# Optimization experiments

Measured on AMD Instinct MI355X. Metric: run time of the kernel, lower is better.

Reference implementation:

```python
import jax, jax.numpy as jnp
import numpy as np

C, PE, L, HEADS = 256, 64, 6, 4
N_GRAPHS, S = 2048, 64            # uniform graphs of S nodes -> dense batch is a reshape
N = N_GRAPHS * S                  # 131072 nodes
E = N * 4                         # 524288 edges
BN_EPS = 1e-5


def _bn(h, g, b):
    # BatchNorm1d, training-mode statistics (biased variance), affine
    m = h.mean(0)
    v = h.var(0)
    return (h - m) / jnp.sqrt(v + BN_EPS) * g + b


def setup_inputs() -> dict:
    key = jax.random.key(0)
    ks = iter(jax.random.split(key, 64))
    def rn(shape, scale=0.05):
        return jax.random.normal(next(ks), shape, dtype=jnp.float32) * scale
    x = jax.random.randint(next(ks), (N, 1), 0, 28)
    pe = jax.random.normal(next(ks), (N, 20), dtype=jnp.float32)
    epg = E // N_GRAPHS
    base = (jnp.arange(E) // epg) * S          # edges stay within their graph
    src = base + jax.random.randint(next(ks), (E,), 0, S)
    dst = base + jax.random.randint(next(ks), (E,), 0, S)
    edge_index = jnp.stack([src, dst])
    edge_attr = jax.random.randint(next(ks), (E,), 0, 4)
    batch = jnp.arange(N) // S
    return dict(
        x=x, pe=pe, edge_index=edge_index, edge_attr=edge_attr, batch=batch,
        node_emb=rn((28, C - PE), 1.0), pe_lin_w=rn((20, PE)), pe_lin_b=jnp.zeros(PE),
        pe_norm_g=jnp.ones(20), pe_norm_b=jnp.zeros(20),
        edge_emb=rn((4, C), 1.0),
        conv_w1=rn((L, C, C)), conv_b1=jnp.zeros((L, C)),
        conv_w2=rn((L, C, C)), conv_b2=jnp.zeros((L, C)),
        attn_in_w=rn((L, C, 3 * C)), attn_in_b=jnp.zeros((L, 3 * C)),
        attn_out_w=rn((L, C, C)), attn_out_b=jnp.zeros((L, C)),
        bn1_g=jnp.ones((L, C)), bn1_b=jnp.zeros((L, C)),
        bn2_g=jnp.ones((L, C)), bn2_b=jnp.zeros((L, C)),
        bn3_g=jnp.ones((L, C)), bn3_b=jnp.zeros((L, C)),
        mlp_w1=rn((L, C, 2 * C)), mlp_b1=jnp.zeros((L, 2 * C)),
        mlp_w2=rn((L, 2 * C, C)), mlp_b2=jnp.zeros((L, C)),
        head_w1=rn((C, C // 2)), head_b1=jnp.zeros(C // 2),
        head_w2=rn((C // 2, C // 4)), head_b2=jnp.zeros(C // 4),
        head_w3=rn((C // 4, 1)), head_b3=jnp.zeros(1),
    )


def reference(x, pe, edge_index, edge_attr, batch, node_emb, pe_lin_w, pe_lin_b,
              pe_norm_g, pe_norm_b, edge_emb, conv_w1, conv_b1, conv_w2, conv_b2,
              attn_in_w, attn_in_b, attn_out_w, attn_out_b,
              bn1_g, bn1_b, bn2_g, bn2_b, bn3_g, bn3_b,
              mlp_w1, mlp_b1, mlp_w2, mlp_b2,
              head_w1, head_b1, head_w2, head_b2, head_w3, head_b3):
    x_pe = _bn(pe, pe_norm_g, pe_norm_b)
    h = jnp.concatenate([node_emb[x[:, 0]], x_pe @ pe_lin_w + pe_lin_b], axis=1)  # [N, C]
    ea = edge_emb[edge_attr]                                                      # [E, C]
    src, dst = edge_index[0], edge_index[1]
    d = C // HEADS
    scale = 1.0 / jnp.sqrt(jnp.float32(d))
    for l in range(L):
        # --- local GINEConv: nn((1+eps)*x_i + sum_j relu(x_j + e_ij)), eps=0 ---
        msg = jax.nn.relu(h[src] + ea)                          # gather + add + relu
        aggr = jax.ops.segment_sum(msg, dst, num_segments=N)    # scatter-add
        z = h + aggr
        hl = jax.nn.relu(z @ conv_w1[l] + conv_b1[l]) @ conv_w2[l] + conv_b2[l]
        hl = _bn(hl + h, bn1_g[l], bn1_b[l])                    # residual + norm1
        # --- global multihead attention on dense batch [G, S, C] ---
        hd = h.reshape(N_GRAPHS, S, C)
        qkv = hd @ attn_in_w[l] + attn_in_b[l]
        q, k, v = jnp.split(qkv, 3, axis=-1)
        q = q.reshape(N_GRAPHS, S, HEADS, d).transpose(0, 2, 1, 3)
        k = k.reshape(N_GRAPHS, S, HEADS, d).transpose(0, 2, 1, 3)
        v = v.reshape(N_GRAPHS, S, HEADS, d).transpose(0, 2, 1, 3)
        a = jax.nn.softmax(jnp.einsum('ghqd,ghkd->ghqk', q, k) * scale, axis=-1)
        o = jnp.einsum('ghqk,ghkd->ghqd', a, v).transpose(0, 2, 1, 3).reshape(N_GRAPHS, S, C)
        o = (o @ attn_out_w[l] + attn_out_b[l]).reshape(N, C)
        ha = _bn(o + h, bn2_g[l], bn2_b[l])                     # residual + norm2
        # --- combine + FFN ---
        out = hl + ha
        ff = jax.nn.relu(out @ mlp_w1[l] + mlp_b1[l]) @ mlp_w2[l] + mlp_b2[l]
        h = _bn(out + ff, bn3_g[l], bn3_b[l])                   # residual + norm3
    pooled = jax.ops.segment_sum(h, batch, num_segments=N_GRAPHS)  # global_add_pool -> [G, C]
    t = jax.nn.relu(pooled @ head_w1 + head_b1)
    t = jax.nn.relu(t @ head_w2 + head_b2)
    return t @ head_w3 + head_b3                                   # [G, 1]
```

## Files before the change

kernel.cpp:

```cpp
#include <hip/hip_runtime.h>

#define N_NODES 131072
#define N_EDGES 524288
#define CCH 256
#define N_GRAPHS_ 2048
#define SEQ 64
#define LAYERS 6

typedef unsigned short US;
typedef __attribute__((ext_vector_type(8))) short v8s;
typedef __attribute__((ext_vector_type(8))) unsigned short v8us;
typedef __attribute__((ext_vector_type(4))) float v4f;

__device__ __forceinline__ float b2f(US u) { return __uint_as_float(((unsigned)u) << 16); }
__device__ __forceinline__ US f2b(float f) {
    unsigned u = __float_as_uint(f);
    return (US)((u + 0x7fff + ((u >> 16) & 1)) >> 16);
}

__device__ float g_stats[512];
__device__ float g_aff1[512];
__device__ float g_aff2[512];
__device__ float g_aff3[512];
__device__ float g_pe[40];
__device__ float g_peaff[40];
__device__ US    g_wt[6 * 655360];
__device__ int   g_csr[N_EDGES];
__device__ int   g_off[N_GRAPHS_ * 65];

__global__ __launch_bounds__(256) void wt_k(const float* __restrict__ cw1, const float* __restrict__ cw2,
                                            const float* __restrict__ aiw, const float* __restrict__ aow,
                                            const float* __restrict__ mw1, const float* __restrict__ mw2) {
    __shared__ float t[64][65];
    int b = blockIdx.x;
    int l = b / 160, r = b % 160;
    const float* src; int ldw, ldk, ctiles; size_t doff;
    if (r < 16)      { src = cw1 + (size_t)l * 65536;  ldw = 256; ldk = 256; ctiles = 4;  doff = 0;      }
    else if (r < 32) { src = cw2 + (size_t)l * 65536;  ldw = 256; ldk = 256; ctiles = 4;  doff = 65536;  r -= 16; }
    else if (r < 80) { src = aiw + (size_t)l * 196608; ldw = 768; ldk = 256; ctiles = 12; doff = 131072; r -= 32; }
    else if (r < 96) { src = aow + (size_t)l * 65536;  ldw = 256; ldk = 256; ctiles = 4;  doff = 327680; r -= 80; }
    else if (r < 128){ src = mw1 + (size_t)l * 131072; ldw = 512; ldk = 256; ctiles = 8;  doff = 393216; r -= 96; }
    else             { src = mw2 + (size_t)l * 131072; ldw = 256; ldk = 512; ctiles = 4;  doff = 524288; r -= 128; }
    int kt = r / ctiles, ct = r % ctiles;
    int k0 = kt * 64, c0 = ct * 64;
    US* dst = g_wt + (size_t)l * 655360 + doff;
    int tid = threadIdx.x;
    int rr = tid >> 4, c4 = (tid & 15) * 4;
    #pragma unroll
    for (int j = 0; j < 4; j++) {
        float4 v = *(const float4*)(src + (size_t)(k0 + rr + j * 16) * ldw + c0 + c4);
        t[rr + j * 16][c4 + 0] = v.x; t[rr + j * 16][c4 + 1] = v.y;
        t[rr + j * 16][c4 + 2] = v.z; t[rr + j * 16][c4 + 3] = v.w;
    }
    __syncthreads();
    #pragma unroll
    for (int j = 0; j < 4; j++) {
        int crow = rr + j * 16;
        ushort4 o;
        o.x = f2b(t[c4 + 0][crow]); o.y = f2b(t[c4 + 1][crow]);
        o.z = f2b(t[c4 + 2][crow]); o.w = f2b(t[c4 + 3][crow]);
        *(ushort4*)(dst + (size_t)(c0 + crow) * ldk + k0 + c4) = o;
    }
}

__global__ __launch_bounds__(256) void csr_k(const int* __restrict__ ei,
                                             const int* __restrict__ attr) {
    __shared__ int deg[64], off[65];
    int g = blockIdx.x, tid = threadIdx.x;
    if (tid < 64) deg[tid] = 0;
    __syncthreads();
    int e = g * 256 + tid;
    int d = ei[N_EDGES + e] - g * 64;
    int slot = atomicAdd(&deg[d], 1);
    __syncthreads();
    if (tid == 0) {
        off[0] = 0;
        for (int i = 0; i < 64; i++) off[i + 1] = off[i] + deg[i];
    }
    __syncthreads();
    g_csr[g * 256 + off[d] + slot] = (ei[e] - g * 64) | (attr[e] << 6);
    if (tid < 65) g_off[g * 65 + tid] = off[tid];
}

__global__ __launch_bounds__(256) void pe_part_k(const float* __restrict__ pe) {
    __shared__ float red[240], red2[240];
    int b = blockIdx.x, tid = threadIdx.x;
    float s = 0.f, s2 = 0.f;
    if (tid < 240) {
        int ch = tid % 20, sub = tid / 20;
        size_t r0 = (size_t)b * 512;
        for (int r = sub; r < 512; r += 12) {
            float v = pe[(r0 + r) * 20 + ch];
            s += v; s2 += v * v;
        }
        red[tid] = s; red2[tid] = s2;
    }
    __syncthreads();
    if (tid < 20) {
        float ts = 0.f, ts2 = 0.f;
        #pragma unroll
        for (int sub = 0; sub < 12; sub++) { ts += red[sub * 20 + tid]; ts2 += red2[sub * 20 + tid]; }
        atomicAdd(&g_pe[tid], ts);
        atomicAdd(&g_pe[20 + tid], ts2);
    }
}

__global__ __launch_bounds__(64) void pe_fin_k(const float* __restrict__ g,
                                               const float* __restrict__ b) {
    int t = threadIdx.x;
    if (t < 20) {
        float mean = g_pe[t] / (float)N_NODES;
        float var  = g_pe[20 + t] / (float)N_NODES - mean * mean;
        float a = g[t] * rsqrtf(var + 1e-5f);
        g_peaff[t] = a;
        g_peaff[20 + t] = b[t] - mean * a;
        g_pe[t] = 0.f;
        g_pe[20 + t] = 0.f;
    }
}

__global__ __launch_bounds__(256) void embed_k(const int* __restrict__ x,
                                               const float* __restrict__ pe,
                                               const float* __restrict__ node_emb,
                                               const float* __restrict__ plw,
                                               const float* __restrict__ plb,
                                               US* __restrict__ h) {
    int n = blockIdx.x;
    int tid = threadIdx.x;
    int xi = x[n];
    float v;
    if (tid < 192) {
        v = node_emb[xi * 192 + tid];
    } else {
        int j = tid - 192;
        float s = plb[j];
        #pragma unroll
        for (int k = 0; k < 20; k++) {
            float p = pe[(size_t)n * 20 + k] * g_peaff[k] + g_peaff[20 + k];
            s += p * plw[k * 64 + j];
        }
        v = s;
    }
    h[(size_t)n * CCH + tid] = f2b(v);
}

__global__ __launch_bounds__(256) void aggr_z_k(const US* __restrict__ h,
                                                const float* __restrict__ eemb,
                                                US* __restrict__ z) {
    __shared__ US ht[64 * 264];
    __shared__ float em[4 * 260];
    __shared__ int off[65], ce[256];
    int g = blockIdx.x, tid = threadIdx.x;
    for (int v = tid; v < 2048; v += 256) {
        int row = v >> 5, seg = (v & 31) * 8;
        *(v8us*)&ht[row * 264 + seg] = *(const v8us*)(h + (size_t)(g * 64 + row) * 256 + seg);
    }
    for (int i = tid; i < 1024; i += 256)
        em[(i >> 8) * 260 + (i & 255)] = eemb[(i >> 8) * 256 + (i & 255)];
    ce[tid] = g_csr[g * 256 + tid];
    if (tid < 65) off[tid] = g_off[g * 65 + tid];
    __syncthreads();

    int dst = tid >> 2, cq = (tid & 3) * 4;
    float acc[64];
    #pragma unroll
    for (int i = 0; i < 64; i++) acc[i] = 0.f;
    int e1 = off[dst + 1];
    for (int e = off[dst]; e < e1; e++) {
        int val = ce[e];
        int src = val & 63, a = (val >> 6) & 3;
        #pragma unroll
        for (int i = 0; i < 16; i++) {
            int c = cq + i * 16;
            ushort4 hv = *(ushort4*)&ht[src * 264 + c];
            float4 ev = *(float4*)&em[a * 260 + c];
            acc[i * 4 + 0] += fmaxf(b2f(hv.x) + ev.x, 0.f);
            acc[i * 4 + 1] += fmaxf(b2f(hv.y) + ev.y, 0.f);
            acc[i * 4 + 2] += fmaxf(b2f(hv.z) + ev.z, 0.f);
            acc[i * 4 + 3] += fmaxf(b2f(hv.w) + ev.w, 0.f);
        }
    }
    US* zp = z + (size_t)(g * 64 + dst) * 256;
    #pragma unroll
    for (int i = 0; i < 16; i++) {
        int c = cq + i * 16;
        ushort4 hv = *(ushort4*)&ht[dst * 264 + c];
        ushort4 o;
        o.x = f2b(b2f(hv.x) + acc[i * 4 + 0]);
        o.y = f2b(b2f(hv.y) + acc[i * 4 + 1]);
        o.z = f2b(b2f(hv.z) + acc[i * 4 + 2]);
        o.w = f2b(b2f(hv.w) + acc[i * 4 + 3]);
        *(ushort4*)(zp + c) = o;
    }
}

template<int NG, bool STATS>
__global__ __launch_bounds__(256, 2) void gemm_mfma_k(const US* __restrict__ A,
                                                      size_t woff, int ldk,
                                                      int w0, int w1, int w2, int w3,
                                                      const float* __restrict__ bias,
                                                      const US* __restrict__ res,
                                                      US* __restrict__ Y, int mode) {
    const US* __restrict__ Wt = g_wt + woff;
    __shared__ __align__(16) US As[128 * 40];
    __shared__ __align__(16) US Bs[NG * 64 * 40];
    int tid = threadIdx.x;
    size_t row0 = (size_t)blockIdx.x * 128;
    int w = tid >> 6, l = tid & 63;

    int sb_c = tid >> 2, sb_ko = (tid & 3) * 8;
    int a_off0 = (w * 32 + (l & 15)) * 40 + (l >> 4) * 8;
    int a_off1 = a_off0 + 16 * 40;
    int b_off  = (l & 15) * 40 + (l >> 4) * 8;

    const US* aptr0 = A + (row0 + sb_c) * 256 + sb_ko;
    const US* aptr1 = aptr0 + 64 * 256;

    v4f acc[2][NG * 4];
    #pragma unroll
    for (int i = 0; i < 2; i++)
        #pragma unroll
        for (int t = 0; t < NG * 4; t++) acc[i][t] = (v4f){0.f, 0.f, 0.f, 0.f};

    v8us pa0 = *(const v8us*)aptr0;
    v8us pa1 = *(const v8us*)aptr1;
    v8us pb[NG];
    #pragma unroll
    for (int p = 0; p < NG; p++) {
        int wb = (p == 0) ? w0 : (p == 1) ? w1 : (p == 2) ? w2 : w3;
        pb[p] = *(const v8us*)(Wt + (size_t)(wb + sb_c) * ldk + sb_ko);
    }

    for (int kc = 0; kc < 8; kc++) {
        *(v8us*)&As[sb_c * 40 + sb_ko] = pa0;
        *(v8us*)&As[(sb_c + 64) * 40 + sb_ko] = pa1;
        #pragma unroll
        for (int p = 0; p < NG; p++)
            *(v8us*)&Bs[(p * 64 + sb_c) * 40 + sb_ko] = pb[p];
        __syncthreads();
        if (kc < 7) {
            int kn = (kc + 1) * 32;
            pa0 = *(const v8us*)(aptr0 + kn);
            pa1 = *(const v8us*)(aptr1 + kn);
            #pragma unroll
            for (int p = 0; p < NG; p++) {
                int wb = (p == 0) ? w0 : (p == 1) ? w1 : (p == 2) ? w2 : w3;
                pb[p] = *(const v8us*)(Wt + (size_t)(wb + sb_c) * ldk + kn + sb_ko);
            }
        }
        v8s a0 = *(v8s*)&As[a_off0];
        v8s a1 = *(v8s*)&As[a_off1];
        #pragma unroll
        for (int t = 0; t < NG * 4; t++) {
            v8s bf = *(v8s*)&Bs[b_off + t * 640];
            acc[0][t] = __builtin_amdgcn_mfma_f32_16x16x32_bf16(a0, bf, acc[0][t], 0, 0, 0);
            acc[1][t] = __builtin_amdgcn_mfma_f32_16x16x32_bf16(a1, bf, acc[1][t], 0, 0, 0);
        }
        __syncthreads();
    }

    int col_l = l & 15;
    int rs = (l >> 4) * 4;
    float cs[NG * 4], cs2[NG * 4];
    if (STATS) {
        #pragma unroll
        for (int t = 0; t < NG * 4; t++) { cs[t] = 0.f; cs2[t] = 0.f; }
    }
    #pragma unroll
    for (int i = 0; i < 2; i++) {
        #pragma unroll
        for (int t = 0; t < NG * 4; t++) {
            int grp = t >> 2;
            int wb = (grp == 0) ? w0 : (grp == 1) ? w1 : (grp == 2) ? w2 : w3;
            int c = t * 16 + col_l;
            float bv = bias ? bias[wb + (t & 3) * 16 + col_l] : 0.f;
            #pragma unroll
            for (int r = 0; r < 4; r++) {
                size_t rr = row0 + w * 32 + i * 16 + rs + r;
                float v = acc[i][t][r] + bv;
                if (mode == 1) v = fmaxf(v, 0.f);
                if (mode == 2) v += b2f(res[rr * 256 + c]);
                if (STATS) { cs[t] += v; cs2[t] += v * v; }
                Y[rr * 256 + c] = f2b(v);
            }
        }
    }
    if (STATS) {
        #pragma unroll
        for (int t = 0; t < NG * 4; t++) {
            cs[t]  += __shfl_xor(cs[t], 16);  cs[t]  += __shfl_xor(cs[t], 32);
            cs2[t] += __shfl_xor(cs2[t], 16); cs2[t] += __shfl_xor(cs2[t], 32);
        }
        float* sred = (float*)As;
        if ((l >> 4) == 0) {
            #pragma unroll
            for (int t = 0; t < NG * 4; t++) {
                sred[w * 256 + t * 16 + col_l] = cs[t];
                sred[1024 + w * 256 + t * 16 + col_l] = cs2[t];
            }
        }
        __syncthreads();
        int c = tid;
        if (c < NG * 64) {
            float s  = sred[c] + sred[256 + c] + sred[512 + c] + sred[768 + c];
            float s2 = sred[1024 + c] + sred[1280 + c] + sred[1536 + c] + sred[1792 + c];
            atomicAdd(&g_stats[c], s);
            atomicAdd(&g_stats[CCH + c], s2);
        }
    }
}

__global__ __launch_bounds__(64) void attn_k(const US* __restrict__ qkv,
                                             US* __restrict__ o) {
    __shared__ __align__(16) US Ps[64 * 72];
    __shared__ __align__(16) US Vt[64 * 72];
    int g = blockIdx.x, l = threadIdx.x;
    int li = l & 15, hi8 = (l >> 4) * 8, hi4 = (l >> 4) * 4;
    const US* base = qkv + (size_t)g * 64 * 256;

    {
        v8us vv[8];
        #pragma unroll
        for (int jv = 0; jv < 8; jv++)
            vv[jv] = *(const v8us*)(base + l * 256 + 128 + jv * 8);
        #pragma unroll
        for (int jv = 0; jv < 8; jv++)
            #pragma unroll
            for (int e = 0; e < 8; e++)
                Vt[(jv * 8 + e) * 72 + l] = vv[jv][e];
    }

    v8s Qf[4][2], Kf[4][2];
    #pragma unroll
    for (int t = 0; t < 4; t++)
        #pragma unroll
        for (int ds = 0; ds < 2; ds++) {
            Qf[t][ds] = *(const v8s*)(base + (t * 16 + li) * 256 + ds * 32 + hi8);
            Kf[t][ds] = *(const v8s*)(base + (t * 16 + li) * 256 + 64 + ds * 32 + hi8);
        }

    v4f S[4][4];
    #pragma unroll
    for (int qt = 0; qt < 4; qt++)
        #pragma unroll
        for (int kt = 0; kt < 4; kt++) {
            v4f a = (v4f){0.f, 0.f, 0.f, 0.f};
            a = __builtin_amdgcn_mfma_f32_16x16x32_bf16(Qf[qt][0], Kf[kt][0], a, 0, 0, 0);
            a = __builtin_amdgcn_mfma_f32_16x16x32_bf16(Qf[qt][1], Kf[kt][1], a, 0, 0, 0);
            S[qt][kt] = a;
        }

    #pragma unroll
    for (int qt = 0; qt < 4; qt++)
        #pragma unroll
        for (int r = 0; r < 4; r++) {
            float mx = -1e30f;
            #pragma unroll
            for (int kt = 0; kt < 4; kt++) {
                S[qt][kt][r] *= 0.125f;
                mx = fmaxf(mx, S[qt][kt][r]);
            }
            mx = fmaxf(mx, __shfl_xor(mx, 1));
            mx = fmaxf(mx, __shfl_xor(mx, 2));
            mx = fmaxf(mx, __shfl_xor(mx, 4));
            mx = fmaxf(mx, __shfl_xor(mx, 8));
            float sum = 0.f;
            #pragma unroll
            for (int kt = 0; kt < 4; kt++) {
                float e = __expf(S[qt][kt][r] - mx);
                S[qt][kt][r] = e;
                sum += e;
            }
            sum += __shfl_xor(sum, 1);
            sum += __shfl_xor(sum, 2);
            sum += __shfl_xor(sum, 4);
            sum += __shfl_xor(sum, 8);
            float inv = 1.f / sum;
            #pragma unroll
            for (int kt = 0; kt < 4; kt++)
                Ps[(qt * 16 + hi4 + r) * 72 + kt * 16 + li] = f2b(S[qt][kt][r] * inv);
        }

    v4f O[4][4];
    #pragma unroll
    for (int qt = 0; qt < 4; qt++)
        #pragma unroll
        for (int jt = 0; jt < 4; jt++) O[qt][jt] = (v4f){0.f, 0.f, 0.f, 0.f};
    #pragma unroll
    for (int ks = 0; ks < 2; ks++) {
        v8s Pf[4], Vf[4];
        #pragma unroll
        for (int qt = 0; qt < 4; qt++)
            Pf[qt] = *(v8s*)&Ps[(qt * 16 + li) * 72 + ks * 32 + hi8];
        #pragma unroll
        for (int jt = 0; jt < 4; jt++)
            Vf[jt] = *(v8s*)&Vt[(jt * 16 + li) * 72 + ks * 32 + hi8];
        #pragma unroll
        for (int qt = 0; qt < 4; qt++)
            #pragma unroll
            for (int jt = 0; jt < 4; jt++)
                O[qt][jt] = __builtin_amdgcn_mfma_f32_16x16x32_bf16(Pf[qt], Vf[jt], O[qt][jt], 0, 0, 0);
    }

    #pragma unroll
    for (int qt = 0; qt < 4; qt++)
        #pragma unroll
        for (int jt = 0; jt < 4; jt++)
            #pragma unroll
            for (int r = 0; r < 4; r++)
                Ps[(qt * 16 + hi4 + r) * 72 + jt * 16 + li] = f2b(O[qt][jt][r]);
    US* ob = o + (size_t)(g * 64 + l) * 256;
    #pragma unroll
    for (int jv = 0; jv < 8; jv++)
        *(v8us*)(ob + jv * 8) = *(v8us*)&Ps[l * 72 + jv * 8];
}

__global__ __launch_bounds__(256) void affine_k(const float* __restrict__ g,
                                                const float* __restrict__ b, int sel) {
    int c = threadIdx.x;
    float mean = g_stats[c] / (float)N_NODES;
    float var  = g_stats[CCH + c] / (float)N_NODES - mean * mean;
    float a = g[c] * rsqrtf(var + 1e-5f);
    float* dst = (sel == 0) ? g_aff1 : (sel == 1) ? g_aff2 : g_aff3;
    dst[c] = a;
    dst[CCH + c] = b[c] - mean * a;
    g_stats[c] = 0.f;
    g_stats[CCH + c] = 0.f;
}

__global__ __launch_bounds__(256) void combine_k(const US* __restrict__ y1,
                                                 const US* __restrict__ y2,
                                                 US* __restrict__ out) {
    size_t idx = (size_t)blockIdx.x * 256 + threadIdx.x;
    size_t stride = (size_t)gridDim.x * 256;
    for (; idx < (size_t)N_NODES * CCH / 8; idx += stride) {
        size_t i = idx * 8;
        int c = (int)(i & 255);
        v8us a = *(const v8us*)(y1 + i);
        v8us b = *(const v8us*)(y2 + i);
        v8us o;
        #pragma unroll
        for (int j = 0; j < 8; j++) {
            float v = b2f(a[j]) * g_aff1[c + j] + g_aff1[CCH + c + j] +
                      b2f(b[j]) * g_aff2[c + j] + g_aff2[CCH + c + j];
            o[j] = f2b(v);
        }
        *(v8us*)(out + i) = o;
    }
}

__global__ __launch_bounds__(256) void apply_k(US* __restrict__ h) {
    size_t idx = (size_t)blockIdx.x * 256 + threadIdx.x;
    size_t stride = (size_t)gridDim.x * 256;
    for (; idx < (size_t)N_NODES * CCH / 8; idx += stride) {
        size_t i = idx * 8;
        int c = (int)(i & 255);
        v8us a = *(const v8us*)(h + i);
        v8us o;
        #pragma unroll
        for (int j = 0; j < 8; j++)
            o[j] = f2b(b2f(a[j]) * g_aff3[c + j] + g_aff3[CCH + c + j]);
        *(v8us*)(h + i) = o;
    }
}

__global__ __launch_bounds__(256) void pool_k(const US* __restrict__ h,
                                              float* __restrict__ pooled) {
    int g = blockIdx.x, c = threadIdx.x;
    float s = 0.f;
    for (int ss = 0; ss < SEQ; ss++) s += b2f(h[((size_t)g * SEQ + ss) * CCH + c]);
    pooled[(size_t)g * CCH + c] = s;
}

__global__ __launch_bounds__(128) void head_k(const float* __restrict__ pooled,
                                              const float* __restrict__ w1, const float* __restrict__ b1,
                                              const float* __restrict__ w2, const float* __restrict__ b2,
                                              const float* __restrict__ w3, const float* __restrict__ b3,
                                              float* __restrict__ outp) {
    __shared__ float p[256], t1[128], t2[64];
    int g = blockIdx.x, tid = threadIdx.x;
    p[tid] = pooled[(size_t)g * CCH + tid];
    p[tid + 128] = pooled[(size_t)g * CCH + 128 + tid];
    __syncthreads();
    float s = b1[tid];
    for (int k = 0; k < 256; k++) s += p[k] * w1[k * 128 + tid];
    t1[tid] = fmaxf(s, 0.f);
    __syncthreads();
    if (tid < 64) {
        float s2 = b2[tid];
        for (int k = 0; k < 128; k++) s2 += t1[k] * w2[k * 64 + tid];
        t2[tid] = fmaxf(s2, 0.f);
    }
    __syncthreads();
    if (tid == 0) {
        float s3 = b3[0];
        for (int k = 0; k < 64; k++) s3 += t2[k] * w3[k];
        outp[g] = s3;
    }
}

extern "C" void kernel_launch(void* const* d_in, const int* in_sizes, int n_in,
                              void* d_out, int out_size, void* d_ws, size_t ws_size,
                              hipStream_t stream) {
    const int*   x         = (const int*)  d_in[0];
    const float* pe        = (const float*)d_in[1];
    const int*   ei        = (const int*)  d_in[2];
    const int*   eattr     = (const int*)  d_in[3];
    const float* node_emb  = (const float*)d_in[5];
    const float* pe_lin_w  = (const float*)d_in[6];
    const float* pe_lin_b  = (const float*)d_in[7];
    const float* pe_norm_g = (const float*)d_in[8];
    const float* pe_norm_b = (const float*)d_in[9];
    const float* edge_emb  = (const float*)d_in[10];
    const float* conv_w1   = (const float*)d_in[11];
    const float* conv_b1   = (const float*)d_in[12];
    const float* conv_w2   = (const float*)d_in[13];
    const float* conv_b2   = (const float*)d_in[14];
    const float* attn_in_w = (const float*)d_in[15];
    const float* attn_in_b = (const float*)d_in[16];
    const float* attn_out_w= (const float*)d_in[17];
    const float* attn_out_b= (const float*)d_in[18];
    const float* bn1_g     = (const float*)d_in[19];
    const float* bn1_b     = (const float*)d_in[20];
    const float* bn2_g     = (const float*)d_in[21];
    const float* bn2_b     = (const float*)d_in[22];
    const float* bn3_g     = (const float*)d_in[23];
    const float* bn3_b     = (const float*)d_in[24];
    const float* mlp_w1    = (const float*)d_in[25];
    const float* mlp_b1    = (const float*)d_in[26];
    const float* mlp_w2    = (const float*)d_in[27];
    const float* mlp_b2    = (const float*)d_in[28];
    const float* head_w1   = (const float*)d_in[29];
    const float* head_b1   = (const float*)d_in[30];
    const float* head_w2   = (const float*)d_in[31];
    const float* head_b2   = (const float*)d_in[32];
    const float* head_w3   = (const float*)d_in[33];
    const float* head_b3   = (const float*)d_in[34];
    (void)in_sizes; (void)n_in; (void)out_size; (void)ws_size;

    char* ws = (char*)d_ws;
    US* h = (US*)(ws);
    US* A = (US*)(ws + 67108864ULL);
    US* B = (US*)(ws + 134217728ULL);
    US* C = (US*)(ws + 201326592ULL);
    float* pooled = (float*)(ws + 67108864ULL);

    wt_k<<<960, 256, 0, stream>>>(conv_w1, conv_w2, attn_in_w, attn_out_w, mlp_w1, mlp_w2);
    csr_k<<<N_GRAPHS_, 256, 0, stream>>>(ei, eattr);
    pe_part_k<<<256, 256, 0, stream>>>(pe);
    pe_fin_k<<<1, 64, 0, stream>>>(pe_norm_g, pe_norm_b);
    embed_k<<<N_NODES, 256, 0, stream>>>(x, pe, node_emb, pe_lin_w, pe_lin_b, h);

    for (int l = 0; l < LAYERS; l++) {
        size_t wl = (size_t)l * 655360;

        aggr_z_k<<<N_GRAPHS_, 256, 0, stream>>>(h, edge_emb, A);
        gemm_mfma_k<4, false><<<1024, 256, 0, stream>>>(A, wl, 256, 0, 64, 128, 192,
                                                        conv_b1 + l * 256, nullptr, B, 1);
        gemm_mfma_k<4, true><<<1024, 256, 0, stream>>>(B, wl + 65536, 256, 0, 64, 128, 192,
                                                       conv_b2 + l * 256, h, C, 2);
        affine_k<<<1, 256, 0, stream>>>(bn1_g + l * 256, bn1_b + l * 256, 0);

        for (int hh = 0; hh < 4; hh++) {
            gemm_mfma_k<3, false><<<1024, 256, 0, stream>>>(h, wl + 131072, 256,
                                                            hh * 64, 256 + hh * 64, 512 + hh * 64, 0,
                                                            attn_in_b + l * 768, nullptr, A, 0);
            attn_k<<<N_GRAPHS_, 64, 0, stream>>>(A, B + hh * 64);
        }
        gemm_mfma_k<4, true><<<1024, 256, 0, stream>>>(B, wl + 327680, 256, 0, 64, 128, 192,
                                                       attn_out_b + l * 256, h, h, 2);
        affine_k<<<1, 256, 0, stream>>>(bn2_g + l * 256, bn2_b + l * 256, 1);

        combine_k<<<2048, 256, 0, stream>>>(C, h, A);
        gemm_mfma_k<4, false><<<1024, 256, 0, stream>>>(A, wl + 393216, 256, 0, 64, 128, 192,
                                                        mlp_b1 + l * 512, nullptr, B, 1);
        gemm_mfma_k<4, false><<<1024, 256, 0, stream>>>(B, wl + 524288, 512, 0, 64, 128, 192,
                                                        mlp_b2 + l * 256, A, C, 2);
        gemm_mfma_k<4, false><<<1024, 256, 0, stream>>>(A, wl + 393216, 256, 256, 320, 384, 448,
                                                        mlp_b1 + l * 512, nullptr, B, 1);
        gemm_mfma_k<4, true><<<1024, 256, 0, stream>>>(B, wl + 524288 + 256, 512, 0, 64, 128, 192,
                                                       nullptr, C, h, 2);
        affine_k<<<1, 256, 0, stream>>>(bn3_g + l * 256, bn3_b + l * 256, 2);
        apply_k<<<2048, 256, 0, stream>>>(h);
    }

    pool_k<<<N_GRAPHS_, 256, 0, stream>>>(h, pooled);
    head_k<<<N_GRAPHS_, 128, 0, stream>>>(pooled, head_w1, head_b1, head_w2, head_b2,
                                          head_w3, head_b3, (float*)d_out);
}
```

Baseline: 5.743 ms.

## Double-buffer GEMM tiles via direct global-to-LDS loads and stage epilogue through LDS

The MFMA GEMM kernel now fills swizzled, double-buffered LDS tiles with global_load_lds, so the next K-chunk loads while the current one computes, with no register round trip. The epilogue writes accumulators to LDS and re-reads them row-wise, giving coalesced 16-byte output and residual accesses. BatchNorm column statistics are now computed from the LDS-staged values. The cost is more barriers in the epilogue and a larger LDS footprint, which could limit occupancy. The stats path assumes all 256 columns are valid, so it only matches the old behaviour when NG is 4.

```diff
diff --git a/kernel.cpp b/kernel.cpp
--- a/kernel.cpp
+++ b/kernel.cpp
@@ -16,6 +16,11 @@
 __device__ __forceinline__ US f2b(float f) {
     unsigned u = __float_as_uint(f);
     return (US)((u + 0x7fff + ((u >> 16) & 1)) >> 16);
+}
+__device__ __forceinline__ void gload16(const US* g, US* l) {
+    __builtin_amdgcn_global_load_lds(
+        (const __attribute__((address_space(1))) unsigned int*)g,
+        (__attribute__((address_space(3))) unsigned int*)l, 16, 0, 0);
 }
 
 __device__ float g_stats[512];
@@ -202,19 +207,24 @@
                                                       const US* __restrict__ res,
                                                       US* __restrict__ Y, int mode) {
     const US* __restrict__ Wt = g_wt + woff;
-    __shared__ __align__(16) US As[128 * 40];
-    __shared__ __align__(16) US Bs[NG * 64 * 40];
+    __shared__ __align__(16) char smem[16384 + 2 * NG * 4096];
+    US* As0 = (US*)smem;
+    US* As1 = (US*)(smem + 8192);
+    US* Bs0 = (US*)(smem + 16384);
+    US* Bs1 = (US*)(smem + 16384 + NG * 4096);
+    float* Es = (float*)smem;
+
     int tid = threadIdx.x;
     size_t row0 = (size_t)blockIdx.x * 128;
     int w = tid >> 6, l = tid & 63;
-
-    int sb_c = tid >> 2, sb_ko = (tid & 3) * 8;
-    int a_off0 = (w * 32 + (l & 15)) * 40 + (l >> 4) * 8;
-    int a_off1 = a_off0 + 16 * 40;
-    int b_off  = (l & 15) * 40 + (l >> 4) * 8;
-
-    const US* aptr0 = A + (row0 + sb_c) * 256 + sb_ko;
-    const US* aptr1 = aptr0 + 64 * 256;
+    int li = l & 15, hi = l >> 4;
+    int sl = hi ^ ((li >> 1) & 3);
+    int srow = l >> 2, sslot = l & 3;
+    int sko = (sslot ^ ((l >> 3) & 3)) * 8;
+
+    int a_off0 = (w * 32 + li) * 32 + sl * 8;
+    int a_off1 = a_off0 + 16 * 32;
+    int b_off  = li * 32 + sl * 8;
 
     v4f acc[2][NG * 4];
     #pragma unroll
@@ -222,91 +232,98 @@
         #pragma unroll
         for (int t = 0; t < NG * 4; t++) acc[i][t] = (v4f){0.f, 0.f, 0.f, 0.f};
 
-    v8us pa0 = *(const v8us*)aptr0;
-    v8us pa1 = *(const v8us*)aptr1;
-    v8us pb[NG];
-    #pragma unroll
-    for (int p = 0; p < NG; p++) {
-        int wb = (p == 0) ? w0 : (p == 1) ? w1 : (p == 2) ? w2 : w3;
-        pb[p] = *(const v8us*)(Wt + (size_t)(wb + sb_c) * ldk + sb_ko);
-    }
-
+    auto stage = [&](int kc, US* Asb, US* Bsb) {
+        int k0 = kc * 32;
+        #pragma unroll
+        for (int j = 0; j < 2; j++) {
+            int q = w * 2 + j;
+            gload16(A + (row0 + q * 16 + srow) * 256 + k0 + sko, Asb + q * 512);
+        }
+        #pragma unroll
+        for (int j = 0; j < NG; j++) {
+            int q = w * NG + j;
+            int col = q * 16 + srow;
+            int grp = col >> 6;
+            int wb = (grp == 0) ? w0 : (grp == 1) ? w1 : (grp == 2) ? w2 : w3;
+            gload16(Wt + (size_t)(wb + (col & 63)) * ldk + k0 + sko, Bsb + q * 512);
+        }
+    };
+
+    stage(0, As0, Bs0);
+    __syncthreads();
     for (int kc = 0; kc < 8; kc++) {
-        *(v8us*)&As[sb_c * 40 + sb_ko] = pa0;
-        *(v8us*)&As[(sb_c + 64) * 40 + sb_ko] = pa1;
-        #pragma unroll
-        for (int p = 0; p < NG; p++)
-            *(v8us*)&Bs[(p * 64 + sb_c) * 40 + sb_ko] = pb[p];
-        __syncthreads();
-        if (kc < 7) {
-            int kn = (kc + 1) * 32;
-            pa0 = *(const v8us*)(aptr0 + kn);
-            pa1 = *(const v8us*)(aptr1 + kn);
-            #pragma unroll
-            for (int p = 0; p < NG; p++) {
-                int wb = (p == 0) ? w0 : (p == 1) ? w1 : (p == 2) ? w2 : w3;
-                pb[p] = *(const v8us*)(Wt + (size_t)(wb + sb_c) * ldk + kn + sb_ko);
-            }
-        }
-        v8s a0 = *(v8s*)&As[a_off0];
-        v8s a1 = *(v8s*)&As[a_off1];
+        US* Asc = (kc & 1) ? As1 : As0;
+        US* Bsc = (kc & 1) ? Bs1 : Bs0;
+        if (kc < 7) stage(kc + 1, (kc & 1) ? As0 : As1, (kc & 1) ? Bs0 : Bs1);
+        v8s a0 = *(v8s*)(Asc + a_off0);
+        v8s a1 = *(v8s*)(Asc + a_off1);
         #pragma unroll
         for (int t = 0; t < NG * 4; t++) {
-            v8s bf = *(v8s*)&Bs[b_off + t * 640];
+            v8s bf = *(v8s*)(Bsc + b_off + t * 512);
             acc[0][t] = __builtin_amdgcn_mfma_f32_16x16x32_bf16(a0, bf, acc[0][t], 0, 0, 0);
             acc[1][t] = __builtin_amdgcn_mfma_f32_16x16x32_bf16(a1, bf, acc[1][t], 0, 0, 0);
         }
         __syncthreads();
     }
 
-    int col_l = l & 15;
-    int rs = (l >> 4) * 4;
-    float cs[NG * 4], cs2[NG * 4];
-    if (STATS) {
-        #pragma unroll
-        for (int t = 0; t < NG * 4; t++) { cs[t] = 0.f; cs2[t] = 0.f; }
-    }
-    #pragma unroll
-    for (int i = 0; i < 2; i++) {
-        #pragma unroll
-        for (int t = 0; t < NG * 4; t++) {
-            int grp = t >> 2;
-            int wb = (grp == 0) ? w0 : (grp == 1) ? w1 : (grp == 2) ? w2 : w3;
-            int c = t * 16 + col_l;
-            float bv = bias ? bias[wb + (t & 3) * 16 + col_l] : 0.f;
-            #pragma unroll
-            for (int r = 0; r < 4; r++) {
-                size_t rr = row0 + w * 32 + i * 16 + rs + r;
-                float v = acc[i][t][r] + bv;
-                if (mode == 1) v = fmaxf(v, 0.f);
-                if (mode == 2) v += b2f(res[rr * 256 + c]);
-                if (STATS) { cs[t] += v; cs2[t] += v * v; }
-                Y[rr * 256 + c] = f2b(v);
+    int er_f = tid >> 3;
+    int lcb = (tid & 7) * 8;
+    float csum = 0.f, csum2 = 0.f;
+    #pragma unroll
+    for (int p = 0; p < 4; p++) {
+        int i = p >> 1, wh = p & 1;
+        if ((w >> 1) == wh) {
+            int er0 = (w & 1) * 16 + hi * 4;
+            #pragma unroll
+            for (int t = 0; t < NG * 4; t++) {
+                int grp = t >> 2;
+                int wb = (grp == 0) ? w0 : (grp == 1) ? w1 : (grp == 2) ? w2 : w3;
+                float bv = bias ? bias[wb + (t & 3) * 16 + li] : 0.f;
+                #pragma unroll
+                for (int r = 0; r < 4; r++) {
+                    float v = acc[i][t][r] + bv;
+                    if (mode == 1) v = fmaxf(v, 0.f);
+                    Es[(er0 + r) * 260 + t * 16 + li] = v;
+                }
             }
         }
-    }
-    if (STATS) {
-        #pragma unroll
-        for (int t = 0; t < NG * 4; t++) {
-            cs[t]  += __shfl_xor(cs[t], 16);  cs[t]  += __shfl_xor(cs[t], 32);
-            cs2[t] += __shfl_xor(cs2[t], 16); cs2[t] += __shfl_xor(cs2[t], 32);
-        }
-        float* sred = (float*)As;
-        if ((l >> 4) == 0) {
-            #pragma unroll
-            for (int t = 0; t < NG * 4; t++) {
-                sred[w * 256 + t * 16 + col_l] = cs[t];
-                sred[1024 + w * 256 + t * 16 + col_l] = cs2[t];
+        __syncthreads();
+        size_t gr = row0 + (size_t)(2 * wh + (er_f >> 4)) * 32 + i * 16 + (er_f & 15);
+        #pragma unroll
+        for (int s = 0; s < NG; s++) {
+            int c = lcb + s * 64;
+            float vs[8];
+            #pragma unroll
+            for (int j = 0; j < 8; j++) vs[j] = Es[er_f * 260 + c + j];
+            if (mode == 2) {
+                v8us rv = *(const v8us*)(res + gr * 256 + c);
+                #pragma unroll
+                for (int j = 0; j < 8; j++) vs[j] += b2f(rv[j]);
             }
+            v8us yv;
+            #pragma unroll
+            for (int j = 0; j < 8; j++) yv[j] = f2b(vs[j]);
+            *(v8us*)(Y + gr * 256 + c) = yv;
+            if constexpr (STATS) {
+                #pragma unroll
+                for (int j = 0; j < 8; j++) Es[er_f * 260 + c + j] = vs[j];
+            }
+        }
+        if constexpr (STATS) {
+            __syncthreads();
+            float s1 = 0.f, s2 = 0.f;
+            #pragma unroll 8
+            for (int r2 = 0; r2 < 32; r2++) {
+                float vv = Es[r2 * 260 + tid];
+                s1 += vv; s2 += vv * vv;
+            }
+            csum += s1; csum2 += s2;
         }
         __syncthreads();
-        int c = tid;
-        if (c < NG * 64) {
-            float s  = sred[c] + sred[256 + c] + sred[512 + c] + sred[768 + c];
-            float s2 = sred[1024 + c] + sred[1280 + c] + sred[1536 + c] + sred[1792 + c];
-            atomicAdd(&g_stats[c], s);
-            atomicAdd(&g_stats[CCH + c], s2);
-        }
+    }
+    if constexpr (STATS) {
+        atomicAdd(&g_stats[tid], csum);
+        atomicAdd(&g_stats[CCH + tid], csum2);
     }
 }
 
```

Result: faster. 5.370 ms (-6.5%).
